# Kernel optimization log

Hardware: AMD Instinct MI355X
Metric: run time of the kernel (lower is better)

The kernel has to match this reference:

```python
import jax, jax.numpy as jnp
import numpy as np

L_DP = 24
N_DP = 12
TAU = 2.0


def setup_inputs() -> dict:
    key = jax.random.key(0)
    ks = jax.random.split(key, 4)
    B, C, T, F = 8, 32, 960, 256
    num_windows = T // L_DP  # 40 (T chosen as multiple of L_DP)
    D = num_windows * F      # 10240
    spikes = jax.random.normal(ks[0], (B, C, T, F), dtype=jnp.float32)
    W1 = jax.random.normal(ks[1], (D, num_windows // 2), dtype=jnp.float32) * (1.0 / np.sqrt(D))
    b1 = jnp.zeros((num_windows // 2,), jnp.float32)
    W2 = jax.random.normal(ks[2], (num_windows // 2, num_windows), dtype=jnp.float32) * (1.0 / np.sqrt(num_windows // 2))
    b2 = jnp.zeros((num_windows,), jnp.float32)
    return {"spikes": spikes, "W1": W1, "b1": b1, "W2": W2, "b2": b2}


def reference(spikes, W1, b1, W2, b2):
    decay = 1.0 - 1.0 / TAU  # leaky-integrator decay = 0.5
    # LINode: affine recurrence v = v*decay + x_t over time axis (axis 2)
    x_seq = jnp.moveaxis(spikes, 2, 0)  # [T, B, C, F]

    def scan_fn(v, x_t):
        v = v * decay + x_t
        return v, v

    _, pots = jax.lax.scan(scan_fn, jnp.zeros_like(x_seq[0]), x_seq)
    potentials = jnp.moveaxis(pots, 0, 2)  # [B, C, T, F]

    v_pooled = jnp.mean(potentials, axis=1)  # [B, T, F]
    B, T, F = v_pooled.shape
    pad_len = (L_DP - T % L_DP) % L_DP
    v_padded = jnp.pad(v_pooled, ((0, 0), (0, pad_len), (0, 0)))
    num_windows = v_padded.shape[1] // L_DP
    v_chunked = v_padded.reshape((B, num_windows, L_DP, F))
    first_part = jnp.mean(v_chunked[:, :, :N_DP, :], axis=2)   # [B, W, F]
    last_part = jnp.mean(v_chunked[:, :, -N_DP:, :], axis=2)   # [B, W, F]
    dp_out = last_part - first_part                             # differential pooling

    dp_flat = dp_out.reshape((B, -1))                           # [B, W*F]
    h = jax.nn.relu(dp_flat @ W1 + b1)                          # [B, W//2]
    ta_weights = jax.nn.softmax(h @ W2 + b2, axis=-1)           # [B, W]
    attended = dp_out * ta_weights[:, :, None]                  # [B, W, F]
    return attended.reshape((B, -1))
```

## Files before the change

### kernel.cpp

```cpp
#include <hip/hip_runtime.h>

#define BB   8
#define CC   32
#define TT   960
#define FF   256
#define LDP  24
#define NDP  12
#define NW   40
#define DFLAT (NW * FF)
#define H1   20
#define WARM 40

__global__ __launch_bounds__(256) void k1_csum(const float4* __restrict__ spikes,
                                               float4* __restrict__ S) {
    const int TF4 = TT * FF / 4;
    int idx = blockIdx.x * 256 + threadIdx.x;
    int b   = idx / TF4;
    int rem = idx - b * TF4;
    const float4* p = spikes + (size_t)b * CC * TF4 + rem;

    float4 a0 = make_float4(0.f, 0.f, 0.f, 0.f);
    float4 a1 = a0, a2 = a0, a3 = a0;
#pragma unroll
    for (int c = 0; c < CC; c += 4) {
        float4 x0 = p[(size_t)(c + 0) * TF4];
        float4 x1 = p[(size_t)(c + 1) * TF4];
        float4 x2 = p[(size_t)(c + 2) * TF4];
        float4 x3 = p[(size_t)(c + 3) * TF4];
        a0.x += x0.x; a0.y += x0.y; a0.z += x0.z; a0.w += x0.w;
        a1.x += x1.x; a1.y += x1.y; a1.z += x1.z; a1.w += x1.w;
        a2.x += x2.x; a2.y += x2.y; a2.z += x2.z; a2.w += x2.w;
        a3.x += x3.x; a3.y += x3.y; a3.z += x3.z; a3.w += x3.w;
    }
    float4 acc = make_float4((a0.x + a1.x) + (a2.x + a3.x),
                             (a0.y + a1.y) + (a2.y + a3.y),
                             (a0.z + a1.z) + (a2.z + a3.z),
                             (a0.w + a1.w) + (a2.w + a3.w));
    S[(size_t)b * TF4 + rem] = acc;
}

__global__ __launch_bounds__(256) void k2_scan(const float4* __restrict__ S,
                                               float4* __restrict__ dp) {
    int wid  = blockIdx.x * 4 + (threadIdx.x >> 6);
    int lane = threadIdx.x & 63;
    int b = wid / NW;
    int w = wid - b * NW;
    int tstart = w * LDP;
    int t0 = tstart - WARM; if (t0 < 0) t0 = 0;
    const float4* Sb = S + (size_t)b * (TT * FF / 4) + lane;

    float4 v    = make_float4(0.f, 0.f, 0.f, 0.f);
    float4 accN = v, accP = v;

    int t = t0;
    for (; t < tstart; ++t) {
        float4 x = Sb[(size_t)t * (FF / 4)];
        v.x = v.x * 0.5f + x.x;  v.y = v.y * 0.5f + x.y;
        v.z = v.z * 0.5f + x.z;  v.w = v.w * 0.5f + x.w;
    }
#pragma unroll
    for (int k = 0; k < NDP; ++k, ++t) {
        float4 x = Sb[(size_t)t * (FF / 4)];
        v.x = v.x * 0.5f + x.x;  v.y = v.y * 0.5f + x.y;
        v.z = v.z * 0.5f + x.z;  v.w = v.w * 0.5f + x.w;
        accN.x += v.x; accN.y += v.y; accN.z += v.z; accN.w += v.w;
    }
#pragma unroll
    for (int k = 0; k < NDP; ++k, ++t) {
        float4 x = Sb[(size_t)t * (FF / 4)];
        v.x = v.x * 0.5f + x.x;  v.y = v.y * 0.5f + x.y;
        v.z = v.z * 0.5f + x.z;  v.w = v.w * 0.5f + x.w;
        accP.x += v.x; accP.y += v.y; accP.z += v.z; accP.w += v.w;
    }
    const float scale = 1.0f / (float)(NDP * CC);
    float4 o = make_float4((accP.x - accN.x) * scale, (accP.y - accN.y) * scale,
                           (accP.z - accN.z) * scale, (accP.w - accN.w) * scale);
    dp[(size_t)(b * NW + w) * (FF / 4) + lane] = o;
}

__global__ __launch_bounds__(256) void k3_mlp(float* __restrict__ dpout,
                                              const float* __restrict__ W1,
                                              const float* __restrict__ b1,
                                              const float* __restrict__ W2,
                                              const float* __restrict__ b2) {
    int b   = blockIdx.x;
    int tid = threadIdx.x;
    float* dp = dpout + (size_t)b * DFLAT;

    __shared__ float red[H1][256];
    __shared__ float ta[NW];

    float acc[H1];
#pragma unroll
    for (int j = 0; j < H1; ++j) acc[j] = 0.f;

    for (int d = tid; d < DFLAT; d += 256) {
        float x = dp[d];
        const float4* w1p = (const float4*)(W1 + (size_t)d * H1);
#pragma unroll
        for (int q = 0; q < 5; ++q) {
            float4 wv = w1p[q];
            acc[4*q+0] = fmaf(x, wv.x, acc[4*q+0]);
            acc[4*q+1] = fmaf(x, wv.y, acc[4*q+1]);
            acc[4*q+2] = fmaf(x, wv.z, acc[4*q+2]);
            acc[4*q+3] = fmaf(x, wv.w, acc[4*q+3]);
        }
    }
#pragma unroll
    for (int j = 0; j < H1; ++j) red[j][tid] = acc[j];
    __syncthreads();
    for (int off = 128; off > 0; off >>= 1) {
        if (tid < off) {
#pragma unroll
            for (int j = 0; j < H1; ++j) red[j][tid] += red[j][tid + off];
        }
        __syncthreads();
    }

    if (tid == 0) {
        float h[H1], z[NW];
#pragma unroll
        for (int j = 0; j < H1; ++j) {
            float v = red[j][0] + b1[j];
            h[j] = v > 0.f ? v : 0.f;
        }
#pragma unroll
        for (int k = 0; k < NW; ++k) z[k] = b2[k];
        for (int j = 0; j < H1; ++j) {
            float hj = h[j];
#pragma unroll
            for (int k = 0; k < NW; ++k) z[k] = fmaf(hj, W2[j * NW + k], z[k]);
        }
        float m = z[0];
        for (int k = 1; k < NW; ++k) m = fmaxf(m, z[k]);
        float s = 0.f;
        for (int k = 0; k < NW; ++k) { z[k] = expf(z[k] - m); s += z[k]; }
        float inv = 1.f / s;
        for (int k = 0; k < NW; ++k) ta[k] = z[k] * inv;
    }
    __syncthreads();

    for (int i = tid; i < DFLAT; i += 256) {
        dp[i] = dp[i] * ta[i >> 8];
    }
}

extern "C" void kernel_launch(void* const* d_in, const int* in_sizes, int n_in,
                              void* d_out, int out_size, void* d_ws, size_t ws_size,
                              hipStream_t stream) {
    const float* spikes = (const float*)d_in[0];
    const float* W1     = (const float*)d_in[1];
    const float* b1     = (const float*)d_in[2];
    const float* W2     = (const float*)d_in[3];
    const float* b2     = (const float*)d_in[4];
    float* out = (float*)d_out;
    float* S   = (float*)d_ws;

    k1_csum<<<dim3(BB * TT * FF / 4 / 256), dim3(256), 0, stream>>>(
        (const float4*)spikes, (float4*)S);
    k2_scan<<<dim3(80), dim3(256), 0, stream>>>(
        (const float4*)S, (float4*)out);
    k3_mlp<<<dim3(BB), dim3(256), 0, stream>>>(out, W1, b1, W2, b2);
}
```

Before: 392.5 us.

## Fuse scan and MLP into one per-batch kernel; nontemporal loads in channel sum

Merges the windowed scan and the MLP/softmax/scale stages into a single kernel with one 1024-thread block per batch. The differential-pooled values stay in shared memory instead of a global round trip, which also removes one kernel launch. The reductions now use wavefront shuffles, and the softmax runs on one wave with one lane per output instead of on a single thread. Separately, the channel-sum kernel uses nontemporal vector loads for the streamed input. The scan now runs on only 8 blocks instead of 80, which cuts parallelism for that stage.

```diff
diff --git a/kernel.cpp b/kernel.cpp
--- a/kernel.cpp
+++ b/kernel.cpp
@@ -1,4 +1,5 @@
 #include <hip/hip_runtime.h>
+#include <math.h>
 
 #define BB   8
 #define CC   32
@@ -11,91 +12,82 @@
 #define H1   20
 #define WARM 40
 
-__global__ __launch_bounds__(256) void k1_csum(const float4* __restrict__ spikes,
-                                               float4* __restrict__ S) {
+typedef float float4n __attribute__((ext_vector_type(4)));
+
+__global__ __launch_bounds__(256) void k1_csum(const float4n* __restrict__ spikes,
+                                               float4n* __restrict__ S) {
     const int TF4 = TT * FF / 4;
     int idx = blockIdx.x * 256 + threadIdx.x;
     int b   = idx / TF4;
     int rem = idx - b * TF4;
-    const float4* p = spikes + (size_t)b * CC * TF4 + rem;
+    const float4n* p = spikes + (size_t)b * CC * TF4 + rem;
 
-    float4 a0 = make_float4(0.f, 0.f, 0.f, 0.f);
-    float4 a1 = a0, a2 = a0, a3 = a0;
+    float4n a0 = (float4n)0.f, a1 = (float4n)0.f,
+            a2 = (float4n)0.f, a3 = (float4n)0.f;
 #pragma unroll
     for (int c = 0; c < CC; c += 4) {
-        float4 x0 = p[(size_t)(c + 0) * TF4];
-        float4 x1 = p[(size_t)(c + 1) * TF4];
-        float4 x2 = p[(size_t)(c + 2) * TF4];
-        float4 x3 = p[(size_t)(c + 3) * TF4];
-        a0.x += x0.x; a0.y += x0.y; a0.z += x0.z; a0.w += x0.w;
-        a1.x += x1.x; a1.y += x1.y; a1.z += x1.z; a1.w += x1.w;
-        a2.x += x2.x; a2.y += x2.y; a2.z += x2.z; a2.w += x2.w;
-        a3.x += x3.x; a3.y += x3.y; a3.z += x3.z; a3.w += x3.w;
+        float4n x0 = __builtin_nontemporal_load(&p[(size_t)(c + 0) * TF4]);
+        float4n x1 = __builtin_nontemporal_load(&p[(size_t)(c + 1) * TF4]);
+        float4n x2 = __builtin_nontemporal_load(&p[(size_t)(c + 2) * TF4]);
+        float4n x3 = __builtin_nontemporal_load(&p[(size_t)(c + 3) * TF4]);
+        a0 += x0; a1 += x1; a2 += x2; a3 += x3;
     }
-    float4 acc = make_float4((a0.x + a1.x) + (a2.x + a3.x),
-                             (a0.y + a1.y) + (a2.y + a3.y),
-                             (a0.z + a1.z) + (a2.z + a3.z),
-                             (a0.w + a1.w) + (a2.w + a3.w));
-    S[(size_t)b * TF4 + rem] = acc;
+    S[(size_t)b * TF4 + rem] = (a0 + a1) + (a2 + a3);
 }
 
-__global__ __launch_bounds__(256) void k2_scan(const float4* __restrict__ S,
-                                               float4* __restrict__ dp) {
-    int wid  = blockIdx.x * 4 + (threadIdx.x >> 6);
-    int lane = threadIdx.x & 63;
-    int b = wid / NW;
-    int w = wid - b * NW;
-    int tstart = w * LDP;
-    int t0 = tstart - WARM; if (t0 < 0) t0 = 0;
+__global__ __launch_bounds__(1024) void k23_scan_mlp(
+        const float4* __restrict__ S, float* __restrict__ out,
+        const float* __restrict__ W1, const float* __restrict__ b1,
+        const float* __restrict__ W2, const float* __restrict__ b2) {
+    int b    = blockIdx.x;
+    int tid  = threadIdx.x;
+    int wave = tid >> 6;
+    int lane = tid & 63;
+
+    __shared__ float dp_s[DFLAT];
+    __shared__ float red[16][H1];
+    __shared__ float ta[NW];
+
     const float4* Sb = S + (size_t)b * (TT * FF / 4) + lane;
-
-    float4 v    = make_float4(0.f, 0.f, 0.f, 0.f);
-    float4 accN = v, accP = v;
-
-    int t = t0;
-    for (; t < tstart; ++t) {
-        float4 x = Sb[(size_t)t * (FF / 4)];
-        v.x = v.x * 0.5f + x.x;  v.y = v.y * 0.5f + x.y;
-        v.z = v.z * 0.5f + x.z;  v.w = v.w * 0.5f + x.w;
+    const float scale = 1.0f / (float)(NDP * CC);
+    for (int w = wave; w < NW; w += 16) {
+        int tstart = w * LDP;
+        int t0 = tstart - WARM; if (t0 < 0) t0 = 0;
+        float4 v    = make_float4(0.f, 0.f, 0.f, 0.f);
+        float4 accN = v, accP = v;
+        int t = t0;
+        for (; t < tstart; ++t) {
+            float4 x = Sb[(size_t)t * (FF / 4)];
+            v.x = v.x * 0.5f + x.x;  v.y = v.y * 0.5f + x.y;
+            v.z = v.z * 0.5f + x.z;  v.w = v.w * 0.5f + x.w;
+        }
+#pragma unroll
+        for (int k = 0; k < NDP; ++k, ++t) {
+            float4 x = Sb[(size_t)t * (FF / 4)];
+            v.x = v.x * 0.5f + x.x;  v.y = v.y * 0.5f + x.y;
+            v.z = v.z * 0.5f + x.z;  v.w = v.w * 0.5f + x.w;
+            accN.x += v.x; accN.y += v.y; accN.z += v.z; accN.w += v.w;
+        }
+#pragma unroll
+        for (int k = 0; k < NDP; ++k, ++t) {
+            float4 x = Sb[(size_t)t * (FF / 4)];
+            v.x = v.x * 0.5f + x.x;  v.y = v.y * 0.5f + x.y;
+            v.z = v.z * 0.5f + x.z;  v.w = v.w * 0.5f + x.w;
+            accP.x += v.x; accP.y += v.y; accP.z += v.z; accP.w += v.w;
+        }
+        float4 o = make_float4((accP.x - accN.x) * scale,
+                               (accP.y - accN.y) * scale,
+                               (accP.z - accN.z) * scale,
+                               (accP.w - accN.w) * scale);
+        ((float4*)dp_s)[w * (FF / 4) + lane] = o;
     }
-#pragma unroll
-    for (int k = 0; k < NDP; ++k, ++t) {
-        float4 x = Sb[(size_t)t * (FF / 4)];
-        v.x = v.x * 0.5f + x.x;  v.y = v.y * 0.5f + x.y;
-        v.z = v.z * 0.5f + x.z;  v.w = v.w * 0.5f + x.w;
-        accN.x += v.x; accN.y += v.y; accN.z += v.z; accN.w += v.w;
-    }
-#pragma unroll
-    for (int k = 0; k < NDP; ++k, ++t) {
-        float4 x = Sb[(size_t)t * (FF / 4)];
-        v.x = v.x * 0.5f + x.x;  v.y = v.y * 0.5f + x.y;
-        v.z = v.z * 0.5f + x.z;  v.w = v.w * 0.5f + x.w;
-        accP.x += v.x; accP.y += v.y; accP.z += v.z; accP.w += v.w;
-    }
-    const float scale = 1.0f / (float)(NDP * CC);
-    float4 o = make_float4((accP.x - accN.x) * scale, (accP.y - accN.y) * scale,
-                           (accP.z - accN.z) * scale, (accP.w - accN.w) * scale);
-    dp[(size_t)(b * NW + w) * (FF / 4) + lane] = o;
-}
-
-__global__ __launch_bounds__(256) void k3_mlp(float* __restrict__ dpout,
-                                              const float* __restrict__ W1,
-                                              const float* __restrict__ b1,
-                                              const float* __restrict__ W2,
-                                              const float* __restrict__ b2) {
-    int b   = blockIdx.x;
-    int tid = threadIdx.x;
-    float* dp = dpout + (size_t)b * DFLAT;
-
-    __shared__ float red[H1][256];
-    __shared__ float ta[NW];
+    __syncthreads();
 
     float acc[H1];
 #pragma unroll
     for (int j = 0; j < H1; ++j) acc[j] = 0.f;
-
-    for (int d = tid; d < DFLAT; d += 256) {
-        float x = dp[d];
+    for (int d = tid; d < DFLAT; d += 1024) {
+        float x = dp_s[d];
         const float4* w1p = (const float4*)(W1 + (size_t)d * H1);
 #pragma unroll
         for (int q = 0; q < 5; ++q) {
@@ -107,42 +99,43 @@
         }
     }
 #pragma unroll
-    for (int j = 0; j < H1; ++j) red[j][tid] = acc[j];
-    __syncthreads();
-    for (int off = 128; off > 0; off >>= 1) {
-        if (tid < off) {
+    for (int j = 0; j < H1; ++j) {
+        float v = acc[j];
 #pragma unroll
-            for (int j = 0; j < H1; ++j) red[j][tid] += red[j][tid + off];
-        }
-        __syncthreads();
-    }
-
-    if (tid == 0) {
-        float h[H1], z[NW];
-#pragma unroll
-        for (int j = 0; j < H1; ++j) {
-            float v = red[j][0] + b1[j];
-            h[j] = v > 0.f ? v : 0.f;
-        }
-#pragma unroll
-        for (int k = 0; k < NW; ++k) z[k] = b2[k];
-        for (int j = 0; j < H1; ++j) {
-            float hj = h[j];
-#pragma unroll
-            for (int k = 0; k < NW; ++k) z[k] = fmaf(hj, W2[j * NW + k], z[k]);
-        }
-        float m = z[0];
-        for (int k = 1; k < NW; ++k) m = fmaxf(m, z[k]);
-        float s = 0.f;
-        for (int k = 0; k < NW; ++k) { z[k] = expf(z[k] - m); s += z[k]; }
-        float inv = 1.f / s;
-        for (int k = 0; k < NW; ++k) ta[k] = z[k] * inv;
+        for (int off = 32; off > 0; off >>= 1) v += __shfl_down(v, off);
+        if (lane == 0) red[wave][j] = v;
     }
     __syncthreads();
 
-    for (int i = tid; i < DFLAT; i += 256) {
-        dp[i] = dp[i] * ta[i >> 8];
+    if (wave == 0) {
+        float h_own = 0.f;
+        if (lane < H1) {
+#pragma unroll
+            for (int w = 0; w < 16; ++w) h_own += red[w][lane];
+            h_own += b1[lane];
+            h_own = h_own > 0.f ? h_own : 0.f;
+        }
+        float z = -INFINITY;
+        if (lane < NW) z = b2[lane];
+#pragma unroll
+        for (int j = 0; j < H1; ++j) {
+            float hj = __shfl(h_own, j);
+            if (lane < NW) z = fmaf(hj, W2[j * NW + lane], z);
+        }
+        float m = z;
+#pragma unroll
+        for (int off = 32; off > 0; off >>= 1) m = fmaxf(m, __shfl_xor(m, off));
+        float e = (lane < NW) ? expf(z - m) : 0.f;
+        float s = e;
+#pragma unroll
+        for (int off = 32; off > 0; off >>= 1) s += __shfl_xor(s, off);
+        if (lane < NW) ta[lane] = e / s;
     }
+    __syncthreads();
+
+    float* ob = out + (size_t)b * DFLAT;
+    for (int i = tid; i < DFLAT; i += 1024)
+        ob[i] = dp_s[i] * ta[i >> 8];
 }
 
 extern "C" void kernel_launch(void* const* d_in, const int* in_sizes, int n_in,
@@ -157,8 +150,7 @@
     float* S   = (float*)d_ws;
 
     k1_csum<<<dim3(BB * TT * FF / 4 / 256), dim3(256), 0, stream>>>(
-        (const float4*)spikes, (float4*)S);
-    k2_scan<<<dim3(80), dim3(256), 0, stream>>>(
-        (const float4*)S, (float4*)out);
-    k3_mlp<<<dim3(BB), dim3(256), 0, stream>>>(out, W1, b1, W2, b2);
+        (const float4n*)spikes, (float4n*)S);
+    k23_scan_mlp<<<dim3(BB), dim3(1024), 0, stream>>>(
+        (const float4*)S, out, W1, b1, W2, b2);
 }
```

New measurement: 382.4 us. 1.03x faster.
